# Kernel optimization log

Hardware: AMD Instinct MI355X
Metric: run time of the kernel (lower is better)

## Reference

```python
import jax, jax.numpy as jnp
import numpy as np

# FFM: 20 fields x 500 features each, k=16
NUM_FIELDS = 20
FIELD_SIZE = 500
TOTAL_FEATURES = NUM_FIELDS * FIELD_SIZE  # 10000
K = 16
BATCH = 4096


def setup_inputs() -> dict:
    key = jax.random.key(0)
    kx, kw, kv = jax.random.split(key, 3)
    x = jax.random.uniform(kx, (BATCH, TOTAL_FEATURES), dtype=jnp.float32)
    w = jax.random.normal(kw, (TOTAL_FEATURES, 1), dtype=jnp.float32)
    v = jax.random.normal(kv, (NUM_FIELDS, TOTAL_FEATURES, K), dtype=jnp.float32)
    return {"x": x, "w": w, "v": v}


def reference(x, w, v):
    B = x.shape[0]
    F, S, k = NUM_FIELDS, FIELD_SIZE, K
    # linear term: [B, 1]
    linear = x @ w
    # group features by field (fields are contiguous, equal-sized)
    xr = x.reshape(B, F, S)            # [b, field i, feat within field]
    vr = v.reshape(F, F, S, k)         # [field g (other), field i, feat, k]
    # E[b, g, i, :] = sum over features of field i of x * v[g]
    # i.e. field-i embedding specialized for interaction with field g
    E = jnp.einsum('bis,gisk->bgik', xr, vr)  # [B, F, F, K]
    # pairwise term: sum_{i<j} <E[b, j, i], E[b, i, j]>
    T = jnp.einsum('bjik,bijk->bij', E, E)    # [B, F, F]
    mask = jnp.triu(jnp.ones((F, F), dtype=bool), 1)
    pair = jnp.sum(jnp.where(mask, T, 0.0), axis=(1, 2))[:, None]  # [B, 1]
    return linear + pair
```

## Files before the change

### kernel.cpp

```cpp
#include <hip/hip_runtime.h>
#include <stdint.h>


#define NF 20
#define FS 500
#define TFEAT 10000
#define KD 16
#define NCOL 336
#define NFRG 21
#define KP 512
#define NB 4096
#define ROWE (NF * NCOL)

typedef __bf16 bf16x8 __attribute__((ext_vector_type(8)));
typedef __bf16 bf16x2 __attribute__((ext_vector_type(2)));
typedef float  f32x4  __attribute__((ext_vector_type(4)));
typedef unsigned int u32x4 __attribute__((ext_vector_type(4)));

typedef __attribute__((address_space(1))) const void* as1cv;
typedef __attribute__((address_space(3))) void* as3v;

__device__ inline void gload_lds16(const void* g, void* l) {
  __builtin_amdgcn_global_load_lds((as1cv)g, (as3v)l, 16, 0, 0);
}

__global__ __launch_bounds__(256) void prep_vt(const float* __restrict__ v,
                                               const float* __restrict__ w,
                                               __bf16* __restrict__ VtS) {
  const int i = blockIdx.x / NFRG;
  const int q = blockIdx.x % NFRG;
  const int tdx = threadIdx.x;
  __shared__ float lv[FS * 17];
  if (q < NF) {
    const int k = tdx & 15, sb = tdx >> 4;
    const float* vb = v + ((size_t)q * TFEAT + (size_t)i * FS) * KD;
    for (int it = 0; it < 32; ++it) {
      int s = it * 16 + sb;
      if (s < FS) lv[s * 17 + k] = vb[(size_t)s * KD + k];
    }
    __syncthreads();
  }
  const float* wf = w + (size_t)i * FS;
  __bf16* base = VtS + ((size_t)i * 16 * NFRG + q) * 512;
  for (int it = 0; it < 4; ++it) {
    int p = it * 256 + tdx;
    int t = p >> 6, l = p & 63;
    int r = l >> 2;
    int kk = t * 32 + (((l & 3) ^ ((l >> 3) & 3)) << 3);
    bf16x8 h;
#pragma unroll
    for (int e = 0; e < 8; ++e) {
      int s = kk + e;
      float val = 0.f;
      if (s < FS) {
        if (q < NF) val = lv[s * 17 + r];
        else if (r == 0) val = wf[s];
      }
      h[e] = (__bf16)val;
    }
    *(bf16x8*)(base + (size_t)t * (NFRG * 512) + l * 8) = h;
  }
}

__global__ __launch_bounds__(256, 3) void k1_gemm(
    const float* __restrict__ x, const __bf16* __restrict__ VtS,
    __bf16* __restrict__ E2, int chunk_base, int tiles) {
  __shared__ __bf16 As[2][64][32];
  __shared__ __bf16 Bs[2][NCOL * 32];

  int bid = blockIdx.x;
  const int nwg = gridDim.x;
  if ((nwg & 7) == 0) {
    int cpx = nwg >> 3;
    bid = (bid & 7) * cpx + (bid >> 3);
  }
  const int i  = bid / tiles;
  const int tb = bid % tiles;
  const int tid = threadIdx.x;
  const int lane = tid & 63, wid = tid >> 6;
  const int b0 = chunk_base + tb * 64;

  const int arow = tid >> 2;
  const int ac16 = (tid & 3) * 16;
  const int ah  = (tid & 3) >> 1;
  const int gh0 = (2 * (tid & 3)) & 3;
  const int rsw = (arow >> 1) & 3;
  const float* xrow = x + (size_t)(b0 + arow) * TFEAT + i * FS;
  const __bf16* VtSi = VtS + (size_t)i * 16 * NFRG * 512 + lane * 8;

  auto issueB = [&](int t) {
#pragma unroll
    for (int jj = 0; jj < 6; ++jj) {
      int q = wid + 4 * jj;
      if (q < NFRG) {
        gload_lds16(VtSi + ((size_t)(2 * t) * NFRG + q) * 512,
                    (void*)&Bs[0][q * 512]);
        gload_lds16(VtSi + ((size_t)(2 * t + 1) * NFRG + q) * 512,
                    (void*)&Bs[1][q * 512]);
      }
    }
  };

  f32x4 arA[4], arB[4];
  auto aload = [&](int t, f32x4* r) {
#pragma unroll
    for (int j = 0; j < 4; ++j) {
      int c = t * 64 + ac16 + j * 4;
      if (c > 496) c = 496;
      r[j] = *(const f32x4*)(xrow + c);
    }
  };
  auto astore = [&](const f32x4* r) {
    bf16x8 h0, h1;
#pragma unroll
    for (int e = 0; e < 4; ++e) {
      h0[e] = (__bf16)r[0][e]; h0[4 + e] = (__bf16)r[1][e];
      h1[e] = (__bf16)r[2][e]; h1[4 + e] = (__bf16)r[3][e];
    }
    *(bf16x8*)(&As[ah][arow][((gh0)     ^ rsw) * 8]) = h0;
    *(bf16x8*)(&As[ah][arow][((gh0 + 1) ^ rsw) * 8]) = h1;
  };

  const int nfr = wid ? 5 : 6;
  const int Fbase = wid ? (1 + wid * 5) : 0;
  const int ar = lane & 15, akc = lane >> 4;

  f32x4 acc[4][6];
#pragma unroll
  for (int m = 0; m < 4; ++m)
#pragma unroll
    for (int nf = 0; nf < 6; ++nf) acc[m][nf] = (f32x4){0.f, 0.f, 0.f, 0.f};

  aload(0, arA);
  issueB(0);
  astore(arA);
  __builtin_amdgcn_sched_barrier(0);
  aload(1, arB);
  __builtin_amdgcn_sched_barrier(0);
  asm volatile("s_waitcnt vmcnt(4) lgkmcnt(0)" ::: "memory");
  __builtin_amdgcn_s_barrier();

#pragma unroll
  for (int t = 0; t < 8; ++t) {
#pragma unroll
    for (int ks = 0; ks < 2; ++ks) {
      bf16x8 af[4];
#pragma unroll
      for (int m = 0; m < 4; ++m) {
        int row = m * 16 + ar;
        int pch = akc ^ ((row >> 1) & 3);
        af[m] = *(const bf16x8*)(&As[ks][row][pch * 8]);
      }
#pragma unroll
      for (int nf = 0; nf < 6; ++nf)
        if (nf < nfr) {
          int n_ = (Fbase + nf) * 16 + ar;
          int pc = akc ^ ((n_ >> 1) & 3);
          bf16x8 bfr = *(const bf16x8*)&Bs[ks][n_ * 32 + pc * 8];
#pragma unroll
          for (int m = 0; m < 4; ++m)
            acc[m][nf] = __builtin_amdgcn_mfma_f32_16x16x32_bf16(af[m], bfr,
                                                                 acc[m][nf], 0, 0, 0);
        }
    }
    if (t < 7) {
      __builtin_amdgcn_s_barrier();
      issueB(t + 1);
      if (t & 1) astore(arA); else astore(arB);
      __builtin_amdgcn_sched_barrier(0);
      if (t < 6) {
        if (t & 1) aload(t + 2, arB); else aload(t + 2, arA);
      }
      __builtin_amdgcn_sched_barrier(0);
      if (t < 6)
        asm volatile("s_waitcnt vmcnt(4) lgkmcnt(0)" ::: "memory");
      else
        asm volatile("s_waitcnt vmcnt(0) lgkmcnt(0)" ::: "memory");
      __builtin_amdgcn_s_barrier();
    }
  }

  const int lr4 = akc * 4, lcol = lane & 15;
#pragma unroll
  for (int m = 0; m < 4; ++m)
#pragma unroll
    for (int nf = 0; nf < 6; ++nf)
      if (nf < nfr) {
        int n = (Fbase + nf) * 16 + lcol;
#pragma unroll
        for (int r = 0; r < 4; ++r) {
          int bl = tb * 64 + m * 16 + lr4 + r;
          E2[(size_t)bl * ROWE + i * NCOL + n] = (__bf16)acc[m][nf][r];
        }
      }
}

__global__ __launch_bounds__(256) void k2_pair(
    const __bf16* __restrict__ E2, float* __restrict__ out, int chunk_base) {
  __shared__ __align__(16) unsigned shw[4][3360];
  const int tid = threadIdx.x, lane = tid & 63, wid = tid >> 6;
  const int bl = blockIdx.x * 4 + wid;
  const unsigned* src = (const unsigned*)(E2 + (size_t)bl * ROWE);
  for (int it = 0; it < 14; ++it) {
    int idx = it * 64 + lane;
    if (idx < 840) {
      u32x4 val = *(const u32x4*)(src + (size_t)idx * 4);
      *(u32x4*)&shw[wid][idx * 4] = val;
    }
  }
  __syncthreads();
  const __bf16* sh = (const __bf16*)shw[wid];
  const int k = lane & 15, g = lane >> 4;
  float sum = 0.f;
  for (int i = g; i < NF; i += 4)
    for (int j = i + 1; j < NF; ++j)
      sum += (float)sh[i * NCOL + j * 16 + k] * (float)sh[j * NCOL + i * 16 + k];
  if (lane < NF) sum += (float)sh[lane * NCOL + 320];
#pragma unroll
  for (int off = 32; off; off >>= 1) sum += __shfl_xor(sum, off);
  if (lane == 0) out[chunk_base + bl] = sum;
}

extern "C" void kernel_launch(void* const* d_in, const int* in_sizes, int n_in,
                              void* d_out, int out_size, void* d_ws, size_t ws_size,
                              hipStream_t stream) {
  const float* x = (const float*)d_in[0];
  const float* w = (const float*)d_in[1];
  const float* v = (const float*)d_in[2];
  float* out = (float*)d_out;
  char* ws = (char*)d_ws;

  const size_t vt_bytes = (size_t)NF * 16 * NFRG * 512 * 2;
  __bf16* VtS = (__bf16*)ws;
  __bf16* E2 = (__bf16*)(ws + vt_bytes);

  size_t eavail = (ws_size > vt_bytes) ? ws_size - vt_bytes : 0;
  int Bc = NB;
  while (Bc > 64 && (size_t)Bc * ROWE * 2 > eavail) Bc >>= 1;

  prep_vt<<<NF * NFRG, 256, 0, stream>>>(v, w, VtS);
  for (int cb = 0; cb < NB; cb += Bc) {
    int tiles = Bc / 64;
    k1_gemm<<<NF * tiles, 256, 0, stream>>>(x, VtS, E2, cb, tiles);
    k2_pair<<<Bc / 4, 256, 0, stream>>>(E2, out, cb);
  }
}
```

Baseline: 75.76 us.

## Load GEMM B fragments directly into registers and use 8 waves per block

The k1 GEMM no longer stages the V/w operand in shared memory through global_load_lds. Each wave now loads its own pre-laid-out bf16x8 B fragments straight from global memory into registers, double-buffered across the two k-halves. Blocks grow to 512 threads (8 waves, 3 or 2 column fragments each), which lowers per-wave accumulator count and raises occupancy. The A tile uses a padded, unswizzled shared layout, and the prep kernel drops its swizzle to match. This removes B's shared-memory traffic and the heavy LDS footprint, but each wave now issues its own global/L2 reads for B instead of sharing one staged copy per block.

```diff
diff --git a/kernel.cpp b/kernel.cpp
--- a/kernel.cpp
+++ b/kernel.cpp
@@ -8,7 +8,6 @@
 #define KD 16
 #define NCOL 336
 #define NFRG 21
-#define KP 512
 #define NB 4096
 #define ROWE (NF * NCOL)
 
@@ -16,13 +15,6 @@
 typedef __bf16 bf16x2 __attribute__((ext_vector_type(2)));
 typedef float  f32x4  __attribute__((ext_vector_type(4)));
 typedef unsigned int u32x4 __attribute__((ext_vector_type(4)));
-
-typedef __attribute__((address_space(1))) const void* as1cv;
-typedef __attribute__((address_space(3))) void* as3v;
-
-__device__ inline void gload_lds16(const void* g, void* l) {
-  __builtin_amdgcn_global_load_lds((as1cv)g, (as3v)l, 16, 0, 0);
-}
 
 __global__ __launch_bounds__(256) void prep_vt(const float* __restrict__ v,
                                                const float* __restrict__ w,
@@ -46,7 +38,7 @@
     int p = it * 256 + tdx;
     int t = p >> 6, l = p & 63;
     int r = l >> 2;
-    int kk = t * 32 + (((l & 3) ^ ((l >> 3) & 3)) << 3);
+    int kk = t * 32 + (l & 3) * 8;
     bf16x8 h;
 #pragma unroll
     for (int e = 0; e < 8; ++e) {
@@ -62,11 +54,10 @@
   }
 }
 
-__global__ __launch_bounds__(256, 3) void k1_gemm(
+__global__ __launch_bounds__(512, 4) void k1_gemm(
     const float* __restrict__ x, const __bf16* __restrict__ VtS,
     __bf16* __restrict__ E2, int chunk_base, int tiles) {
-  __shared__ __bf16 As[2][64][32];
-  __shared__ __bf16 Bs[2][NCOL * 32];
+  __shared__ __bf16 As[2][64][72];
 
   int bid = blockIdx.x;
   const int nwg = gridDim.x;
@@ -80,103 +71,97 @@
   const int lane = tid & 63, wid = tid >> 6;
   const int b0 = chunk_base + tb * 64;
 
-  const int arow = tid >> 2;
-  const int ac16 = (tid & 3) * 16;
-  const int ah  = (tid & 3) >> 1;
-  const int gh0 = (2 * (tid & 3)) & 3;
-  const int rsw = (arow >> 1) & 3;
+  const int arow = tid >> 3;
+  const int acol = (tid & 7) * 8;
   const float* xrow = x + (size_t)(b0 + arow) * TFEAT + i * FS;
-  const __bf16* VtSi = VtS + (size_t)i * 16 * NFRG * 512 + lane * 8;
-
-  auto issueB = [&](int t) {
-#pragma unroll
-    for (int jj = 0; jj < 6; ++jj) {
-      int q = wid + 4 * jj;
-      if (q < NFRG) {
-        gload_lds16(VtSi + ((size_t)(2 * t) * NFRG + q) * 512,
-                    (void*)&Bs[0][q * 512]);
-        gload_lds16(VtSi + ((size_t)(2 * t + 1) * NFRG + q) * 512,
-                    (void*)&Bs[1][q * 512]);
-      }
-    }
+
+  const int ar = lane & 15, akc = lane >> 4;
+  const int Fbase = (wid < 5) ? 3 * wid : 15 + 2 * (wid - 5);
+  const int nfr   = (wid < 5) ? 3 : 2;
+  const __bf16* vlane = VtS + (size_t)i * 16 * NFRG * 512
+                      + (size_t)(ar * 4 + akc) * 8
+                      + (size_t)Fbase * 512;
+
+  f32x4 arA[2], arB[2];
+  auto aload = [&](int t, f32x4* r) {
+    int c0 = t * 64 + acol;     if (c0 > 496) c0 = 496;
+    int c1 = t * 64 + acol + 4; if (c1 > 496) c1 = 496;
+    r[0] = *(const f32x4*)(xrow + c0);
+    r[1] = *(const f32x4*)(xrow + c1);
   };
-
-  f32x4 arA[4], arB[4];
-  auto aload = [&](int t, f32x4* r) {
-#pragma unroll
-    for (int j = 0; j < 4; ++j) {
-      int c = t * 64 + ac16 + j * 4;
-      if (c > 496) c = 496;
-      r[j] = *(const f32x4*)(xrow + c);
-    }
+  auto astore = [&](int buf, const f32x4* r) {
+    bf16x8 h;
+#pragma unroll
+    for (int e = 0; e < 4; ++e) {
+      h[e] = (__bf16)r[0][e]; h[4 + e] = (__bf16)r[1][e];
+    }
+    *(bf16x8*)(&As[buf][arow][acol]) = h;
   };
-  auto astore = [&](const f32x4* r) {
-    bf16x8 h0, h1;
-#pragma unroll
-    for (int e = 0; e < 4; ++e) {
-      h0[e] = (__bf16)r[0][e]; h0[4 + e] = (__bf16)r[1][e];
-      h1[e] = (__bf16)r[2][e]; h1[4 + e] = (__bf16)r[3][e];
-    }
-    *(bf16x8*)(&As[ah][arow][((gh0)     ^ rsw) * 8]) = h0;
-    *(bf16x8*)(&As[ah][arow][((gh0 + 1) ^ rsw) * 8]) = h1;
+  auto loadB = [&](int t32, bf16x8* bq) {
+#pragma unroll
+    for (int nf = 0; nf < 3; ++nf)
+      if (nf < nfr)
+        bq[nf] = *(const bf16x8*)(vlane + ((size_t)t32 * NFRG + nf) * 512);
   };
 
-  const int nfr = wid ? 5 : 6;
-  const int Fbase = wid ? (1 + wid * 5) : 0;
-  const int ar = lane & 15, akc = lane >> 4;
-
-  f32x4 acc[4][6];
+  f32x4 acc[4][3];
 #pragma unroll
   for (int m = 0; m < 4; ++m)
 #pragma unroll
-    for (int nf = 0; nf < 6; ++nf) acc[m][nf] = (f32x4){0.f, 0.f, 0.f, 0.f};
+    for (int nf = 0; nf < 3; ++nf) acc[m][nf] = (f32x4){0.f, 0.f, 0.f, 0.f};
+  bf16x8 bqA[3], bqB[3];
 
   aload(0, arA);
-  issueB(0);
-  astore(arA);
-  __builtin_amdgcn_sched_barrier(0);
+  astore(0, arA);
   aload(1, arB);
-  __builtin_amdgcn_sched_barrier(0);
-  asm volatile("s_waitcnt vmcnt(4) lgkmcnt(0)" ::: "memory");
+  loadB(0, bqA);
+  asm volatile("s_waitcnt lgkmcnt(0)" ::: "memory");
   __builtin_amdgcn_s_barrier();
 
-#pragma unroll
   for (int t = 0; t < 8; ++t) {
-#pragma unroll
-    for (int ks = 0; ks < 2; ++ks) {
+    const int cur = t & 1;
+    loadB(2 * t + 1, bqB);
+    __builtin_amdgcn_sched_barrier(0);
+    if (t < 7) {
+      if (t & 1) astore(cur ^ 1, arA); else astore(cur ^ 1, arB);
+    }
+    if (t < 6) {
+      if (t & 1) aload(t + 2, arB); else aload(t + 2, arA);
+    }
+    __builtin_amdgcn_sched_barrier(0);
+
+    {
       bf16x8 af[4];
 #pragma unroll
-      for (int m = 0; m < 4; ++m) {
-        int row = m * 16 + ar;
-        int pch = akc ^ ((row >> 1) & 3);
-        af[m] = *(const bf16x8*)(&As[ks][row][pch * 8]);
-      }
-#pragma unroll
-      for (int nf = 0; nf < 6; ++nf)
-        if (nf < nfr) {
-          int n_ = (Fbase + nf) * 16 + ar;
-          int pc = akc ^ ((n_ >> 1) & 3);
-          bf16x8 bfr = *(const bf16x8*)&Bs[ks][n_ * 32 + pc * 8];
+      for (int m = 0; m < 4; ++m)
+        af[m] = *(const bf16x8*)(&As[cur][m * 16 + ar][akc * 8]);
+#pragma unroll
+      for (int nf = 0; nf < 3; ++nf)
+        if (nf < nfr)
 #pragma unroll
           for (int m = 0; m < 4; ++m)
-            acc[m][nf] = __builtin_amdgcn_mfma_f32_16x16x32_bf16(af[m], bfr,
+            acc[m][nf] = __builtin_amdgcn_mfma_f32_16x16x32_bf16(af[m], bqA[nf],
                                                                  acc[m][nf], 0, 0, 0);
-        }
+    }
+    __builtin_amdgcn_sched_barrier(0);
+    if (t < 7) loadB(2 * t + 2, bqA);
+    __builtin_amdgcn_sched_barrier(0);
+    {
+      bf16x8 af[4];
+#pragma unroll
+      for (int m = 0; m < 4; ++m)
+        af[m] = *(const bf16x8*)(&As[cur][m * 16 + ar][32 + akc * 8]);
+#pragma unroll
+      for (int nf = 0; nf < 3; ++nf)
+        if (nf < nfr)
+#pragma unroll
+          for (int m = 0; m < 4; ++m)
+            acc[m][nf] = __builtin_amdgcn_mfma_f32_16x16x32_bf16(af[m], bqB[nf],
+                                                                 acc[m][nf], 0, 0, 0);
     }
     if (t < 7) {
+      asm volatile("s_waitcnt lgkmcnt(0)" ::: "memory");
       __builtin_amdgcn_s_barrier();
-      issueB(t + 1);
-      if (t & 1) astore(arA); else astore(arB);
-      __builtin_amdgcn_sched_barrier(0);
-      if (t < 6) {
-        if (t & 1) aload(t + 2, arB); else aload(t + 2, arA);
-      }
-      __builtin_amdgcn_sched_barrier(0);
-      if (t < 6)
-        asm volatile("s_waitcnt vmcnt(4) lgkmcnt(0)" ::: "memory");
-      else
-        asm volatile("s_waitcnt vmcnt(0) lgkmcnt(0)" ::: "memory");
-      __builtin_amdgcn_s_barrier();
     }
   }
 
@@ -184,7 +169,7 @@
 #pragma unroll
   for (int m = 0; m < 4; ++m)
 #pragma unroll
-    for (int nf = 0; nf < 6; ++nf)
+    for (int nf = 0; nf < 3; ++nf)
       if (nf < nfr) {
         int n = (Fbase + nf) * 16 + lcol;
 #pragma unroll
@@ -241,7 +226,7 @@
   prep_vt<<<NF * NFRG, 256, 0, stream>>>(v, w, VtS);
   for (int cb = 0; cb < NB; cb += Bc) {
     int tiles = Bc / 64;
-    k1_gemm<<<NF * tiles, 256, 0, stream>>>(x, VtS, E2, cb, tiles);
+    k1_gemm<<<NF * tiles, 512, 0, stream>>>(x, VtS, E2, cb, tiles);
     k2_pair<<<Bc / 4, 256, 0, stream>>>(E2, out, cb);
   }
 }
```

New measurement: 72.89 us. -3.8%, faster.
